# Kernel tuning notes

Hardware: AMD Instinct MI355X
Metric: run time of the kernel (lower is better)

Reference implementation:

```python
import jax, jax.numpy as jnp
import numpy as np

DIM = 3072      # model dim (Qwen-Image)
HEADS = 24
HD = 128        # head dim; inner = HEADS*HD = 3072
INNER = HEADS * HD
FF = 4 * DIM    # 12288
S_IMG = 1024
S_TXT = 256
S_TOT = S_IMG + S_TXT
B = 1
EPS = 1e-6
SCALE_SHIFT = 1.0


def setup_inputs() -> dict:
    key = jax.random.key(0)
    ks = iter(jax.random.split(key, 64))
    W = 0.02

    def nrm(shape, s=W):
        return jax.random.normal(next(ks), shape, dtype=jnp.float32) * s

    # RoPE tables for the joint (txt first, then img) sequence, interleaved layout
    pos = jnp.arange(S_TOT, dtype=jnp.float32)
    inv = 1.0 / (10000.0 ** (jnp.arange(HD // 2, dtype=jnp.float32) / (HD // 2)))
    ang = pos[:, None] * inv[None, :]                       # [S, HD/2]
    rope_cos = jnp.repeat(jnp.cos(ang), 2, axis=-1)         # [S, HD]
    rope_sin = jnp.repeat(jnp.sin(ang), 2, axis=-1)

    inp = {
        "hidden_states": jax.random.normal(next(ks), (B, S_IMG, DIM), dtype=jnp.float32),
        "encoder_hidden_states": jax.random.normal(next(ks), (B, S_TXT, DIM), dtype=jnp.float32),
        "temb": jax.random.normal(next(ks), (B, DIM), dtype=jnp.float32),
        "rope_cos": rope_cos,
        "rope_sin": rope_sin,
        # modulation (AWQW4A16Linear equivalent)
        "img_mod_w": nrm((6 * DIM, DIM)), "img_mod_b": nrm((6 * DIM,)),
        "txt_mod_w": nrm((6 * DIM, DIM)), "txt_mod_b": nrm((6 * DIM,)),
        # attention (SVDQW4A4Linear equivalents)
        "qkv_w": nrm((3 * INNER, DIM)), "qkv_b": nrm((3 * INNER,)),
        "add_qkv_w": nrm((3 * INNER, DIM)), "add_qkv_b": nrm((3 * INNER,)),
        "norm_q_g": jnp.ones((HD,), jnp.float32), "norm_k_g": jnp.ones((HD,), jnp.float32),
        "norm_added_q_g": jnp.ones((HD,), jnp.float32), "norm_added_k_g": jnp.ones((HD,), jnp.float32),
        "to_out_w": nrm((DIM, INNER)), "to_out_b": nrm((DIM,)),
        "to_add_out_w": nrm((DIM, INNER)), "to_add_out_b": nrm((DIM,)),
        # MLPs
        "img_mlp_w1": nrm((FF, DIM)), "img_mlp_b1": nrm((FF,)),
        "img_mlp_w2": nrm((DIM, FF)), "img_mlp_b2": nrm((DIM,)),
        "txt_mlp_w1": nrm((FF, DIM)), "txt_mlp_b1": nrm((FF,)),
        "txt_mlp_w2": nrm((DIM, FF)), "txt_mlp_b2": nrm((DIM,)),
    }
    return inp


def _lin(x, w, b):
    return jnp.matmul(x, w.T) + b


def _ln(x):  # LayerNorm, no affine, eps=1e-6
    mu = jnp.mean(x, axis=-1, keepdims=True)
    var = jnp.mean(jnp.square(x - mu), axis=-1, keepdims=True)
    return (x - mu) * jax.lax.rsqrt(var + EPS)


def _rms(x, g):  # per-head RMSNorm over last dim (HD)
    ms = jnp.mean(jnp.square(x), axis=-1, keepdims=True)
    return x * jax.lax.rsqrt(ms + EPS) * g


def _rope(x, cos, sin):  # x: [B,S,H,D], cos/sin: [S,D], interleaved rotate
    x1 = x[..., 0::2]
    x2 = x[..., 1::2]
    xr = jnp.stack([-x2, x1], axis=-1).reshape(x.shape)
    return x * cos[None, :, None, :] + xr * sin[None, :, None, :]


def _reorder_mod(m):
    # view(B,-1,6).transpose(1,2).reshape(B,-1): de-interleave 6 modulation vecs
    b = m.shape[0]
    return m.reshape(b, DIM, 6).transpose(0, 2, 1).reshape(b, 6 * DIM)


def _modulate(x, mod):
    shift, scale, gate = jnp.split(mod, 3, axis=-1)
    return x * (scale + SCALE_SHIFT)[:, None, :] + shift[:, None, :], gate[:, None, :]


def _mlp(x, w1, b1, w2, b2):  # GELU(tanh) MLP
    h = jax.nn.gelu(_lin(x, w1, b1), approximate=True)
    return _lin(h, w2, b2)


def reference(hidden_states, encoder_hidden_states, temb, rope_cos, rope_sin,
              img_mod_w, img_mod_b, txt_mod_w, txt_mod_b,
              qkv_w, qkv_b, add_qkv_w, add_qkv_b,
              norm_q_g, norm_k_g, norm_added_q_g, norm_added_k_g,
              to_out_w, to_out_b, to_add_out_w, to_add_out_b,
              img_mlp_w1, img_mlp_b1, img_mlp_w2, img_mlp_b2,
              txt_mlp_w1, txt_mlp_b1, txt_mlp_w2, txt_mlp_b2):
    b = hidden_states.shape[0]

    img_mod = _reorder_mod(_lin(jax.nn.silu(temb), img_mod_w, img_mod_b))
    txt_mod = _reorder_mod(_lin(jax.nn.silu(temb), txt_mod_w, txt_mod_b))
    img_mod1, img_mod2 = jnp.split(img_mod, 2, axis=-1)
    txt_mod1, txt_mod2 = jnp.split(txt_mod, 2, axis=-1)

    img_modulated, img_gate1 = _modulate(_ln(hidden_states), img_mod1)
    txt_modulated, txt_gate1 = _modulate(_ln(encoder_hidden_states), txt_mod1)

    # ---- joint attention ----
    img_q, img_k, img_v = jnp.split(_lin(img_modulated, qkv_w, qkv_b), 3, axis=-1)
    txt_q, txt_k, txt_v = jnp.split(_lin(txt_modulated, add_qkv_w, add_qkv_b), 3, axis=-1)

    def heads(x):  # [B,S,INNER] -> [B,S,H,HD]
        return x.reshape(b, x.shape[1], HEADS, HD)

    img_q = _rms(heads(img_q), norm_q_g)
    img_k = _rms(heads(img_k), norm_k_g)
    txt_q = _rms(heads(txt_q), norm_added_q_g)
    txt_k = _rms(heads(txt_k), norm_added_k_g)

    q = jnp.concatenate([txt_q, img_q], axis=1)  # txt first
    k = jnp.concatenate([txt_k, img_k], axis=1)
    v = jnp.concatenate([heads(txt_v), heads(img_v)], axis=1)

    q = _rope(q, rope_cos, rope_sin)
    k = _rope(k, rope_cos, rope_sin)

    scale = 1.0 / jnp.sqrt(jnp.float32(HD))
    scores = jnp.einsum('bqhd,bkhd->bhqk', q, k) * scale
    probs = jax.nn.softmax(scores, axis=-1)
    attn = jnp.einsum('bhqk,bkhd->bqhd', probs, v).reshape(b, S_TOT, INNER)

    txt_attn = attn[:, :S_TXT, :]
    img_attn = attn[:, S_TXT:, :]
    img_attn = _lin(img_attn, to_out_w, to_out_b)
    txt_attn = _lin(txt_attn, to_add_out_w, to_add_out_b)

    hidden_states = hidden_states + img_gate1 * img_attn
    encoder_hidden_states = encoder_hidden_states + txt_gate1 * txt_attn

    # ---- MLPs ----
    img_m2, img_gate2 = _modulate(_ln(hidden_states), img_mod2)
    hidden_states = hidden_states + img_gate2 * _mlp(img_m2, img_mlp_w1, img_mlp_b1, img_mlp_w2, img_mlp_b2)

    txt_m2, txt_gate2 = _modulate(_ln(encoder_hidden_states), txt_mod2)
    encoder_hidden_states = encoder_hidden_states + txt_gate2 * _mlp(txt_m2, txt_mlp_w1, txt_mlp_b1, txt_mlp_w2, txt_mlp_b2)

    return (encoder_hidden_states, hidden_states)
```

## Files before the change

kernel.cpp:

```cpp
#include <hip/hip_runtime.h>

#define DIMC   3072
#define HEADS  24
#define HD     128
#define FF     12288
#define S_IMG  1024
#define S_TXT  256
#define S_TOT  1280
#define EPSF   1e-6f

typedef __attribute__((ext_vector_type(8))) short bf16x8;
typedef __attribute__((ext_vector_type(4))) float f32x4;
typedef __attribute__((ext_vector_type(4))) float float4v;
typedef __attribute__((ext_vector_type(4))) unsigned int u32x4;

__device__ __forceinline__ unsigned short f2bf(float f) {
    union { float f; unsigned u; } c; c.f = f;
    unsigned u = c.u;
    unsigned r = (u + 0x7fffu + ((u >> 16) & 1u)) >> 16;
    return (unsigned short)r;
}
__device__ __forceinline__ float b2f(unsigned short h) {
    union { unsigned u; float f; } c; c.u = ((unsigned)h) << 16;
    return c.f;
}
__device__ __forceinline__ unsigned packbf(float a, float b) {
    union { float f; unsigned u; } x, y; x.f = a; y.f = b;
    return __builtin_amdgcn_perm(y.u + 0x8000u, x.u + 0x8000u, 0x07060302);
}
__device__ __forceinline__ float gelu_tanh(float v) {
    float u = 1.5957691216057308f * (v + 0.044715f * v * v * v);
    float e = __expf(u);
    float t = 1.0f - 2.0f / (e + 1.0f);
    return 0.5f * v * (1.0f + t);
}

#define GLL16(gsrc, ldst)                                                     \
    __builtin_amdgcn_global_load_lds(                                         \
        (const __attribute__((address_space(1))) void*)(gsrc),                \
        (__attribute__((address_space(3))) void*)(ldst), 16, 0, 0)

struct GemmArgs {
    const unsigned short* A;
    const void* B;
    const float* bias;
    void* out;
    long bOut;
};

template<int EPI>
__global__ __launch_bounds__(512, 2)
void gemm_big(GemmArgs g0, GemmArgs g1, int ysplit,
              int K, int lda, int ldb, int ldout)
{
    __shared__ __align__(16) char smem[131072];
    char* smemA = smem;
    char* smemB = smem + 65536;

    const int tid  = threadIdx.x;
    const int lane = tid & 63;
    const int wave = tid >> 6;
    const int wm = wave >> 2, wc = wave & 3;

    const int by = blockIdx.y;
    const bool second = (by >= ysplit);
    const GemmArgs g = second ? g1 : g0;
    const int bm = (second ? by - ysplit : by) * 256;
    const int bn = blockIdx.x * 256;

    const unsigned short* A = g.A;
    const float* Bf = (const float*)g.B;

    const int rA = lane >> 3;
    const int cA = (lane & 7) ^ rA;
    const int pB = tid & 7;
    const int rB0 = tid >> 3;
    const int swB = (rB0 & 7) << 4;

    float4v breg[4][2];

    auto BLOAD = [&](int t) {
        const float* src = Bf + (long)t * 64 + pB * 8;
        #pragma unroll
        for (int i = 0; i < 4; i++) {
            const float* p = src + (long)(bn + rB0 + i * 64) * ldb;
            breg[i][0] = *(const float4v*)p;
            breg[i][1] = *(const float4v*)(p + 4);
        }
    };
    auto ASTAGE = [&](int buf, int t) {
        const long kof = (long)t * 64 + cA * 8;
        #pragma unroll
        for (int i = 0; i < 4; i++) {
            int r = i * 64 + wave * 8 + rA;
            GLL16(A + (long)(bm + r) * lda + kof,
                  smemA + buf * 32768 + i * 8192 + wave * 1024);
        }
    };
    auto BSTORE = [&](int buf) {
        #pragma unroll
        for (int i = 0; i < 4; i++) {
            int r = rB0 + i * 64;
            u32x4 w;
            w[0] = packbf(breg[i][0][0], breg[i][0][1]);
            w[1] = packbf(breg[i][0][2], breg[i][0][3]);
            w[2] = packbf(breg[i][1][0], breg[i][1][1]);
            w[3] = packbf(breg[i][1][2], breg[i][1][3]);
            *(u32x4*)(smemB + buf * 32768 + r * 128 + ((pB * 16) ^ swB)) = w;
        }
    };

    f32x4 acc[8][4] = {};
    auto COMPUTE = [&](int buf) {
        #pragma unroll
        for (int ks = 0; ks < 2; ks++) {
            const int kb = ks * 64 + (lane >> 4) * 16;
            bf16x8 af[8], bfr[4];
            #pragma unroll
            for (int mi = 0; mi < 8; mi++) {
                int r = wm * 128 + mi * 16 + (lane & 15);
                af[mi] = *(const bf16x8*)(smemA + buf * 32768 + r * 128 + (kb ^ ((r & 7) << 4)));
            }
            #pragma unroll
            for (int ni = 0; ni < 4; ni++) {
                int r = wc * 64 + ni * 16 + (lane & 15);
                bfr[ni] = *(const bf16x8*)(smemB + buf * 32768 + r * 128 + (kb ^ ((r & 7) << 4)));
            }
            #pragma unroll
            for (int mi = 0; mi < 8; mi++)
                #pragma unroll
                for (int ni = 0; ni < 4; ni++)
                    acc[mi][ni] = __builtin_amdgcn_mfma_f32_16x16x32_bf16(
                        af[mi], bfr[ni], acc[mi][ni], 0, 0, 0);
        }
    };

    const int nk = K >> 6;
    BLOAD(0);
    ASTAGE(0, 0);
    BSTORE(0);
    __syncthreads();
    for (int t = 0; t < nk; ++t) {
        const int cur = t & 1;
        if (t + 1 < nk) {
            BLOAD(t + 1);
            ASTAGE(cur ^ 1, t + 1);
        }
        __builtin_amdgcn_sched_barrier(0);
        COMPUTE(cur);
        __builtin_amdgcn_sched_barrier(0);
        if (t + 1 < nk) BSTORE(cur ^ 1);
        __syncthreads();
    }

    unsigned short* outh = (unsigned short*)g.out;
    float*          outf = (float*)g.out;
    #pragma unroll
    for (int mi = 0; mi < 8; mi++) {
        #pragma unroll
        for (int ni = 0; ni < 4; ni++) {
            int n = bn + wc * 64 + ni * 16 + (lane & 15);
            float bv = g.bias ? g.bias[n] : 0.0f;
            #pragma unroll
            for (int r = 0; r < 4; r++) {
                int m = bm + wm * 128 + mi * 16 + (lane >> 4) * 4 + r;
                float v = acc[mi][ni][r] + bv;
                long o = (long)m * ldout + n;
                if constexpr (EPI == 0) outf[o] = v;
                else                    outh[o] = f2bf(gelu_tanh(v));
            }
        }
    }
}

template<int EPI, bool BF16B>
__global__ __launch_bounds__(256)
void gemm_bt(GemmArgs g0, GemmArgs g1, int ysplit,
             int K, int lda, int ldb, int ldout,
             long batchA, long batchB)
{
    __shared__ __align__(16) char smem[65536];
    char* smemA = smem;
    char* smemB = smem + 32768;

    const int tid  = threadIdx.x;
    const int lane = tid & 63;
    const int wave = tid >> 6;
    const int wm = wave >> 1, wc = wave & 1;

    const int by = blockIdx.y;
    const bool second = (by >= ysplit);
    const GemmArgs g = second ? g1 : g0;
    const int bm = (second ? by - ysplit : by) * 128;
    const int bn = blockIdx.x * 128;

    const unsigned short* A = g.A + (long)blockIdx.z * batchA;
    const float* Bf = (const float*)g.B + (long)blockIdx.z * batchB;
    const unsigned short* Bh = (const unsigned short*)g.B + (long)blockIdx.z * batchB;

    const int rA = lane >> 3;
    const int cA = (lane & 7) ^ rA;
    const int pB = tid & 7;
    const int rB0 = tid >> 3;
    const int swB = (rB0 & 7) << 4;

    float4v breg[4][2];

    auto BLOAD = [&](int t) {
        const float* src = Bf + (long)t * 64 + pB * 8;
        #pragma unroll
        for (int i = 0; i < 4; i++) {
            const float* p = src + (long)(bn + rB0 + i * 32) * ldb;
            breg[i][0] = *(const float4v*)p;
            breg[i][1] = *(const float4v*)(p + 4);
        }
    };
    auto STAGE_A = [&](int buf, int t) {
        const long kof = (long)t * 64 + cA * 8;
        #pragma unroll
        for (int i = 0; i < 4; i++) {
            int r = i * 32 + wave * 8 + rA;
            GLL16(A + (long)(bm + r) * lda + kof,
                  smemA + buf * 16384 + i * 4096 + wave * 1024);
        }
    };
    auto STAGE_B16 = [&](int buf, int t) {
        const long kof = (long)t * 64 + cA * 8;
        #pragma unroll
        for (int i = 0; i < 4; i++) {
            int r = i * 32 + wave * 8 + rA;
            GLL16(Bh + (long)(bn + r) * ldb + kof,
                  smemB + buf * 16384 + i * 4096 + wave * 1024);
        }
    };
    auto BSTORE = [&](int buf) {
        #pragma unroll
        for (int i = 0; i < 4; i++) {
            int r = rB0 + i * 32;
            u32x4 w;
            w[0] = packbf(breg[i][0][0], breg[i][0][1]);
            w[1] = packbf(breg[i][0][2], breg[i][0][3]);
            w[2] = packbf(breg[i][1][0], breg[i][1][1]);
            w[3] = packbf(breg[i][1][2], breg[i][1][3]);
            *(u32x4*)(smemB + buf * 16384 + r * 128 + ((pB * 16) ^ swB)) = w;
        }
    };

    f32x4 acc[4][4] = {};
    auto COMPUTE = [&](int buf) {
        #pragma unroll
        for (int ks = 0; ks < 2; ks++) {
            const int kb = ks * 64 + (lane >> 4) * 16;
            bf16x8 af[4], bfr[4];
            #pragma unroll
            for (int mi = 0; mi < 4; mi++) {
                int r = wm * 64 + mi * 16 + (lane & 15);
                af[mi] = *(const bf16x8*)(smemA + buf * 16384 + r * 128 + (kb ^ ((r & 7) << 4)));
            }
            #pragma unroll
            for (int ni = 0; ni < 4; ni++) {
                int r = wc * 64 + ni * 16 + (lane & 15);
                bfr[ni] = *(const bf16x8*)(smemB + buf * 16384 + r * 128 + (kb ^ ((r & 7) << 4)));
            }
            #pragma unroll
            for (int mi = 0; mi < 4; mi++)
                #pragma unroll
                for (int ni = 0; ni < 4; ni++)
                    acc[mi][ni] = __builtin_amdgcn_mfma_f32_16x16x32_bf16(
                        af[mi], bfr[ni], acc[mi][ni], 0, 0, 0);
        }
    };

    const int nk = K >> 6;
    if constexpr (BF16B) {
        STAGE_A(0, 0); STAGE_B16(0, 0);
    } else {
        BLOAD(0); STAGE_A(0, 0); BSTORE(0);
    }
    __syncthreads();
    for (int t = 0; t < nk; ++t) {
        const int cur = t & 1;
        if (t + 1 < nk) {
            if constexpr (BF16B) {
                STAGE_A(cur ^ 1, t + 1); STAGE_B16(cur ^ 1, t + 1);
            } else {
                BLOAD(t + 1); STAGE_A(cur ^ 1, t + 1);
            }
        }
        __builtin_amdgcn_sched_barrier(0);
        COMPUTE(cur);
        __builtin_amdgcn_sched_barrier(0);
        if constexpr (!BF16B) { if (t + 1 < nk) BSTORE(cur ^ 1); }
        __syncthreads();
    }

    unsigned short* outh = (unsigned short*)g.out + (long)blockIdx.z * g.bOut;
    float*          outf = (float*)g.out + (long)blockIdx.z * g.bOut;
    #pragma unroll
    for (int mi = 0; mi < 4; mi++) {
        #pragma unroll
        for (int ni = 0; ni < 4; ni++) {
            int n = bn + wc * 64 + ni * 16 + (lane & 15);
            float bv = g.bias ? g.bias[n] : 0.0f;
            #pragma unroll
            for (int r = 0; r < 4; r++) {
                int m = bm + wm * 64 + mi * 16 + (lane >> 4) * 4 + r;
                float v = acc[mi][ni][r] + bv;
                long o = (long)m * ldout + n;
                if constexpr (EPI == 0)      outf[o] = v;
                else                         outh[o] = f2bf(v);
            }
        }
    }
}

__global__ void silu_k(const float* __restrict__ x, float* __restrict__ out) {
    int i = blockIdx.x * 256 + threadIdx.x;
    if (i < DIMC) { float v = x[i]; out[i] = v / (1.0f + expf(-v)); }
}

__global__ __launch_bounds__(256)
void mod_gemv(const float* __restrict__ st,
              const float* __restrict__ Wimg, const float* __restrict__ bimg,
              const float* __restrict__ Wtxt, const float* __restrict__ btxt,
              float* __restrict__ mimg, float* __restrict__ mtxt)
{
    int wv = threadIdx.x >> 6, lane = threadIdx.x & 63;
    int r = blockIdx.x * 4 + wv;
    const float* W = blockIdx.y ? Wtxt : Wimg;
    const float* b = blockIdx.y ? btxt : bimg;
    float* out = blockIdx.y ? mtxt : mimg;
    const float* row = W + (long)r * DIMC;
    float acc = 0.f;
    #pragma unroll
    for (int j = 0; j < 12; j++) {
        float4v wvv = ((const float4v*)row)[lane + j * 64];
        float4v xv  = ((const float4v*)st)[lane + j * 64];
        acc += wvv[0] * xv[0] + wvv[1] * xv[1] + wvv[2] * xv[2] + wvv[3] * xv[3];
    }
    #pragma unroll
    for (int o = 32; o; o >>= 1) acc += __shfl_xor(acc, o);
    if (lane == 0) {
        int d = r / 6, j6 = r % 6;
        out[j6 * DIMC + d] = acc + b[r];
    }
}

__global__ __launch_bounds__(256)
void ln_mod(const float* __restrict__ x, const float* __restrict__ shift,
            const float* __restrict__ scale, unsigned short* __restrict__ out)
{
    __shared__ float red[8];
    long row = blockIdx.x;
    const float* xr = x + row * DIMC;
    float4v v[3];
    float sum = 0.f, sq = 0.f;
    #pragma unroll
    for (int j = 0; j < 3; j++) {
        v[j] = ((const float4v*)xr)[threadIdx.x + j * 256];
        #pragma unroll
        for (int c = 0; c < 4; c++) { sum += v[j][c]; sq += v[j][c] * v[j][c]; }
    }
    int lane = threadIdx.x & 63, wv = threadIdx.x >> 6;
// ... 37 lines not shown
        float4v q1 = ((const float4v*)(p1 + off))[idx];
        float4v gb = ((const float4v*)pbias)[idx];
        float4v gt = ((const float4v*)gate1)[idx];
        #pragma unroll
        for (int c = 0; c < 4; c++) {
            float val = a[c] + gt[c] * (gb[c] + q0[c] + q1[c]);
            v[j][c] = val; sum += val; sq += val * val;
        }
        ((float4v*)(h1 + off))[idx] = v[j];
    }
    int lane = threadIdx.x & 63, wv = threadIdx.x >> 6;
    #pragma unroll
    for (int o = 32; o; o >>= 1) { sum += __shfl_xor(sum, o); sq += __shfl_xor(sq, o); }
    if (lane == 0) { red[wv] = sum; red[4 + wv] = sq; }
    __syncthreads();
    sum = red[0] + red[1] + red[2] + red[3];
    sq  = red[4] + red[5] + red[6] + red[7];
    float mu = sum / DIMC;
    float rstd = rsqrtf(sq / DIMC - mu * mu + EPSF);
    #pragma unroll
    for (int j = 0; j < 3; j++) {
        int nb = (threadIdx.x + j * 256) * 4;
        #pragma unroll
        for (int c = 0; c < 4; c++) {
            int n = nb + c;
            float y = (v[j][c] - mu) * rstd * (scale2[n] + 1.0f) + shift2[n];
            mA[off + n] = f2bf(y);
        }
    }
}

__global__ __launch_bounds__(256)
void reduce_out(const float* __restrict__ p, long PS,
                const float* __restrict__ h1, const float* __restrict__ wbias,
                const float* __restrict__ gate2, float* __restrict__ out, int n4)
{
    int i = blockIdx.x * 256 + threadIdx.x;
    if (i >= n4) return;
    int n = (i * 4) % DIMC;
    float4v s = ((const float4v*)p)[i];
    float4v s1 = ((const float4v*)(p + PS))[i];
    float4v s2 = ((const float4v*)(p + 2 * PS))[i];
    float4v s3 = ((const float4v*)(p + 3 * PS))[i];
    float4v h = ((const float4v*)h1)[i];
    float4v bv = *(const float4v*)(wbias + n);
    float4v gv = *(const float4v*)(gate2 + n);
    float4v r;
    #pragma unroll
    for (int c = 0; c < 4; c++)
        r[c] = h[c] + gv[c] * (bv[c] + s[c] + s1[c] + s2[c] + s3[c]);
    ((float4v*)out)[i] = r;
}

__global__ __launch_bounds__(64)
void qkv_post(const float* __restrict__ qkv_img, const float* __restrict__ qkv_txt,
              const float* __restrict__ nqg, const float* __restrict__ nkg,
              const float* __restrict__ naqg, const float* __restrict__ nakg,
              const float* __restrict__ rc, const float* __restrict__ rs,
              unsigned short* __restrict__ q, unsigned short* __restrict__ k,
              unsigned short* __restrict__ vt)
{
    int s = blockIdx.x;
    int h = blockIdx.y;
    int d0 = threadIdx.x;
    const float *src, *gq, *gk;
    if (s < S_TXT) { src = qkv_txt + (long)s * 3 * DIMC; gq = naqg; gk = nakg; }
    else           { src = qkv_img + (long)(s - S_TXT) * 3 * DIMC; gq = nqg; gk = nkg; }

    float q0 = src[h * HD + d0],            q1 = src[h * HD + d0 + 64];
    float k0 = src[DIMC + h * HD + d0],     k1 = src[DIMC + h * HD + d0 + 64];
    float v0 = src[2 * DIMC + h * HD + d0], v1 = src[2 * DIMC + h * HD + d0 + 64];

    float sqq = q0 * q0 + q1 * q1;
    float sqk = k0 * k0 + k1 * k1;
    #pragma unroll
    for (int o = 32; o; o >>= 1) { sqq += __shfl_xor(sqq, o); sqk += __shfl_xor(sqk, o); }
    float rq = rsqrtf(sqq / (float)HD + EPSF);
    float rk = rsqrtf(sqk / (float)HD + EPSF);
    q0 *= rq * gq[d0]; q1 *= rq * gq[d0 + 64];
    k0 *= rk * gk[d0]; k1 *= rk * gk[d0 + 64];

    float qp0 = __shfl_xor(q0, 1), qp1 = __shfl_xor(q1, 1);
    float kp0 = __shfl_xor(k0, 1), kp1 = __shfl_xor(k1, 1);
    float c0 = rc[(long)s * HD + d0], c1 = rc[(long)s * HD + d0 + 64];
    float s0 = rs[(long)s * HD + d0], s1 = rs[(long)s * HD + d0 + 64];
    float sgn = (d0 & 1) ? 1.0f : -1.0f;
    float qo0 = q0 * c0 + sgn * qp0 * s0;
    float qo1 = q1 * c1 + sgn * qp1 * s1;
    float ko0 = k0 * c0 + sgn * kp0 * s0;
    float ko1 = k1 * c1 + sgn * kp1 * s1;

    const float scl = 0.08838834764831845f;
    long qkbase = ((long)h * S_TOT + s) * HD;
    q[qkbase + d0]      = f2bf(qo0 * scl);
    q[qkbase + d0 + 64] = f2bf(qo1 * scl);
    k[qkbase + d0]      = f2bf(ko0);
    k[qkbase + d0 + 64] = f2bf(ko1);
    vt[((long)h * HD + d0) * S_TOT + s]        = f2bf(v0);
    vt[((long)h * HD + d0 + 64) * S_TOT + s]   = f2bf(v1);
}

__global__ __launch_bounds__(256)
void softmax_k(unsigned short* __restrict__ scores)
{
    long row = (long)blockIdx.x * 4 + (threadIdx.x >> 6);
    int lane = threadIdx.x & 63;
    unsigned short* p = scores + row * S_TOT;
    float v[20];
    float mx = -1e30f;
    #pragma unroll
    for (int j = 0; j < 20; j++) { v[j] = b2f(p[lane + j * 64]); mx = fmaxf(mx, v[j]); }
    #pragma unroll
    for (int o = 32; o; o >>= 1) mx = fmaxf(mx, __shfl_xor(mx, o));
    float sum = 0.f;
    #pragma unroll
    for (int j = 0; j < 20; j++) { v[j] = __expf(v[j] - mx); sum += v[j]; }
    #pragma unroll
    for (int o = 32; o; o >>= 1) sum += __shfl_xor(sum, o);
    float inv = 1.0f / sum;
    #pragma unroll
    for (int j = 0; j < 20; j++) p[lane + j * 64] = f2bf(v[j] * inv);
}

extern "C" void kernel_launch(void* const* d_in, const int* in_sizes, int n_in,
                              void* d_out, int out_size, void* d_ws, size_t ws_size,
                              hipStream_t stream)
{
    const float* hidden   = (const float*)d_in[0];
    const float* enc      = (const float*)d_in[1];
    const float* temb     = (const float*)d_in[2];
    const float* rope_cos = (const float*)d_in[3];
    const float* rope_sin = (const float*)d_in[4];
    const float* img_mod_w = (const float*)d_in[5];
    const float* img_mod_b = (const float*)d_in[6];
    const float* txt_mod_w = (const float*)d_in[7];
    const float* txt_mod_b = (const float*)d_in[8];
    const float* qkv_w     = (const float*)d_in[9];
    const float* qkv_b     = (const float*)d_in[10];
    const float* add_qkv_w = (const float*)d_in[11];
    const float* add_qkv_b = (const float*)d_in[12];
    const float* norm_q_g  = (const float*)d_in[13];
    const float* norm_k_g  = (const float*)d_in[14];
    const float* norm_aq_g = (const float*)d_in[15];
    const float* norm_ak_g = (const float*)d_in[16];
    const float* to_out_w  = (const float*)d_in[17];
    const float* to_out_b  = (const float*)d_in[18];
    const float* to_add_out_w = (const float*)d_in[19];
    const float* to_add_out_b = (const float*)d_in[20];
    const float* img_mlp_w1 = (const float*)d_in[21];
    const float* img_mlp_b1 = (const float*)d_in[22];
    const float* img_mlp_w2 = (const float*)d_in[23];
    const float* img_mlp_b2 = (const float*)d_in[24];
    const float* txt_mlp_w1 = (const float*)d_in[25];
    const float* txt_mlp_b1 = (const float*)d_in[26];
    const float* txt_mlp_w2 = (const float*)d_in[27];
    const float* txt_mlp_b2 = (const float*)d_in[28];

    char* w = (char*)d_ws;
    auto alloc = [&](size_t bytes) { char* p = w; w += (bytes + 255) & ~(size_t)255; return p; };
    float* silu_t  = (float*)alloc(DIMC * 4);
    float* mod_img = (float*)alloc(6 * DIMC * 4);
    float* mod_txt = (float*)alloc(6 * DIMC * 4);
    unsigned short* mA_img = (unsigned short*)alloc((long)S_IMG * DIMC * 2);
    unsigned short* mA_txt = (unsigned short*)alloc((long)S_TXT * DIMC * 2);
    float* qkv_img = (float*)alloc((long)S_IMG * 3 * DIMC * 4);
    float* qkv_txt = (float*)alloc((long)S_TXT * 3 * DIMC * 4);
    unsigned short* qb = (unsigned short*)alloc((long)HEADS * S_TOT * HD * 2);
    unsigned short* kb = (unsigned short*)alloc((long)HEADS * S_TOT * HD * 2);
    unsigned short* vt = (unsigned short*)alloc((long)HEADS * HD * S_TOT * 2);
    unsigned short* scores = (unsigned short*)alloc((long)HEADS * S_TOT * S_TOT * 2);
    unsigned short* attn = (unsigned short*)alloc((long)S_TOT * DIMC * 2);
    float* h1_img = (float*)alloc((long)S_IMG * DIMC * 4);
    float* h1_txt = (float*)alloc((long)S_TXT * DIMC * 4);
    unsigned short* gelu_img = (unsigned short*)alloc((long)S_IMG * FF * 2);
    unsigned short* gelu_txt = (unsigned short*)alloc((long)S_TXT * FF * 2);

    const long PS = (long)S_TOT * DIMC;
    float* part = (float*)scores;
    float* part_img = part;
    float* part_txt = part + (long)S_IMG * DIMC;

    float* out_enc = (float*)d_out;
    float* out_hid = (float*)d_out + (long)S_TXT * DIMC;

    silu_k<<<12, 256, 0, stream>>>(temb, silu_t);
    mod_gemv<<<dim3(4608, 2), 256, 0, stream>>>(silu_t, img_mod_w, img_mod_b,
                                                txt_mod_w, txt_mod_b, mod_img, mod_txt);

    ln_mod<<<S_IMG, 256, 0, stream>>>(hidden, mod_img, mod_img + DIMC, mA_img);
    ln_mod<<<S_TXT, 256, 0, stream>>>(enc, mod_txt, mod_txt + DIMC, mA_txt);

    {
        GemmArgs gi{mA_img, qkv_w, qkv_b, qkv_img, 0};
        GemmArgs gt{mA_txt, add_qkv_w, add_qkv_b, qkv_txt, 0};
        gemm_big<0><<<dim3(36, 5), 512, 0, stream>>>(
            gi, gt, 4, DIMC, DIMC, DIMC, 3 * DIMC);
    }

    qkv_post<<<dim3(S_TOT, HEADS), 64, 0, stream>>>(
        qkv_img, qkv_txt, norm_q_g, norm_k_g, norm_aq_g, norm_ak_g,
        rope_cos, rope_sin, qb, kb, vt);

    {
        GemmArgs gs{qb, kb, nullptr, scores, (long)S_TOT * S_TOT};
        gemm_bt<1, true><<<dim3(10, 10, HEADS), 256, 0, stream>>>(
            gs, gs, 10, HD, HD, HD, S_TOT,
            (long)S_TOT * HD, (long)S_TOT * HD);
    }
    softmax_k<<<(HEADS * S_TOT) / 4, 256, 0, stream>>>(scores);
    {
        GemmArgs gp{scores, vt, nullptr, attn, HD};
        gemm_bt<1, true><<<dim3(1, 10, HEADS), 256, 0, stream>>>(
            gp, gp, 10, S_TOT, S_TOT, S_TOT, DIMC,
            (long)S_TOT * S_TOT, (long)HD * S_TOT);
    }

    {
        GemmArgs gi{attn + (long)S_TXT * DIMC, to_out_w, nullptr, part_img, PS};
        GemmArgs gt{attn, to_add_out_w, nullptr, part_txt, PS};
        gemm_bt<0, false><<<dim3(24, 10, 2), 256, 0, stream>>>(
            gi, gt, 8, 1536, DIMC, DIMC, DIMC, 1536, 1536);
    }

    reduce_ln<<<S_IMG, 256, 0, stream>>>(
        part_img, part_img + PS, to_out_b, hidden,
        mod_img + 2 * DIMC, mod_img + 3 * DIMC, mod_img + 4 * DIMC,
        h1_img, mA_img);
    reduce_ln<<<S_TXT, 256, 0, stream>>>(
        part_txt, part_txt + PS, to_add_out_b, enc,
        mod_txt + 2 * DIMC, mod_txt + 3 * DIMC, mod_txt + 4 * DIMC,
        h1_txt, mA_txt);

    {
        GemmArgs gi{mA_img, img_mlp_w1, img_mlp_b1, gelu_img, 0};
        GemmArgs gt{mA_txt, txt_mlp_w1, txt_mlp_b1, gelu_txt, 0};
        gemm_big<2><<<dim3(48, 5), 512, 0, stream>>>(
            gi, gt, 4, DIMC, DIMC, DIMC, FF);
    }

    {
        GemmArgs gi{gelu_img, img_mlp_w2, nullptr, part_img, PS};
        GemmArgs gt{gelu_txt, txt_mlp_w2, nullptr, part_txt, PS};
        gemm_bt<0, false><<<dim3(24, 10, 4), 256, 0, stream>>>(
            gi, gt, 8, 3072, FF, FF, DIMC, 3072, 3072);
    }
    reduce_out<<<(S_IMG * DIMC / 4 + 255) / 256, 256, 0, stream>>>(
        part_img, PS, h1_img, img_mlp_b2, mod_img + 5 * DIMC, out_hid,
        S_IMG * DIMC / 4);
    reduce_out<<<(S_TXT * DIMC / 4 + 255) / 256, 256, 0, stream>>>(
        part_txt, PS, h1_txt, txt_mlp_b2, mod_txt + 5 * DIMC, out_enc,
        S_TXT * DIMC / 4);
}
```

Before: 765.0 us.

## Swap GEMM operands and stage bf16 output tile through LDS for coalesced stores

```diff
diff --git a/kernel.cpp b/kernel.cpp
--- a/kernel.cpp
+++ b/kernel.cpp
@@ -13,6 +13,7 @@
 typedef __attribute__((ext_vector_type(4))) float f32x4;
 typedef __attribute__((ext_vector_type(4))) float float4v;
 typedef __attribute__((ext_vector_type(4))) unsigned int u32x4;
+typedef __attribute__((ext_vector_type(2))) unsigned int u32x2;
 
 __device__ __forceinline__ unsigned short f2bf(float f) {
     union { float f; unsigned u; } c; c.f = f;
@@ -39,6 +40,149 @@
     __builtin_amdgcn_global_load_lds(                                         \
         (const __attribute__((address_space(1))) void*)(gsrc),                \
         (__attribute__((address_space(3))) void*)(ldst), 16, 0, 0)
+
+struct SwpArgs {
+    const float* W;
+    const unsigned short* X;
+    const float* bias;
+    unsigned short* out;
+};
+
+template<int EPI>
+__global__ __launch_bounds__(512, 2)
+void gemm_swp(SwpArgs g0, SwpArgs g1, int ysplit, int K, int ldout)
+{
+    __shared__ __align__(16) char smem[131072];
+    char* smemW = smem;
+    char* smemX = smem + 65536;
+
+    const int tid  = threadIdx.x;
+    const int lane = tid & 63;
+    const int wave = tid >> 6;
+    const int wm = wave >> 2, wc = wave & 3;
+
+    const int by = blockIdx.y;
+    const bool second = (by >= ysplit);
+    const SwpArgs g = second ? g1 : g0;
+    const int sTile = (second ? by - ysplit : by) * 256;
+    const int bm = blockIdx.x * 256;
+
+    const int pW  = tid & 7;
+    const int rW0 = tid >> 3;
+    const int swW = (rW0 & 7) << 4;
+    const int rX = lane >> 3;
+    const int cX = (lane & 7) ^ rX;
+
+    float4v wreg[4][2];
+
+    auto WLOAD = [&](int t) {
+        const float* src = g.W + (long)t * 64 + pW * 8;
+        #pragma unroll
+        for (int i = 0; i < 4; i++) {
+            const float* p = src + (long)(bm + rW0 + i * 64) * K;
+            wreg[i][0] = *(const float4v*)p;
+            wreg[i][1] = *(const float4v*)(p + 4);
+        }
+    };
+    auto WSTORE = [&](int buf) {
+        #pragma unroll
+        for (int i = 0; i < 4; i++) {
+            int r = rW0 + i * 64;
+            u32x4 w;
+            w[0] = packbf(wreg[i][0][0], wreg[i][0][1]);
+            w[1] = packbf(wreg[i][0][2], wreg[i][0][3]);
+            w[2] = packbf(wreg[i][1][0], wreg[i][1][1]);
+            w[3] = packbf(wreg[i][1][2], wreg[i][1][3]);
+            *(u32x4*)(smemW + buf * 32768 + r * 128 + ((pW * 16) ^ swW)) = w;
+        }
+    };
+    auto XSTAGE = [&](int buf, int t) {
+        const long kof = (long)t * 64 + cX * 8;
+        #pragma unroll
+        for (int i = 0; i < 4; i++) {
+            int r = i * 64 + wave * 8 + rX;
+            GLL16(g.X + (long)(sTile + r) * K + kof,
+                  smemX + buf * 32768 + i * 8192 + wave * 1024);
+        }
+    };
+
+    f32x4 acc[8][4] = {};
+    auto COMPUTE = [&](int buf) {
+        #pragma unroll
+        for (int ks = 0; ks < 2; ks++) {
+            const int kb = ks * 64 + (lane >> 4) * 16;
+            bf16x8 wf[8], xf[4];
+            #pragma unroll
+            for (int mi = 0; mi < 8; mi++) {
+                int r = wm * 128 + mi * 16 + (lane & 15);
+                wf[mi] = *(const bf16x8*)(smemW + buf * 32768 + r * 128 + (kb ^ ((r & 7) << 4)));
+            }
+            #pragma unroll
+            for (int ni = 0; ni < 4; ni++) {
+                int r = wc * 64 + ni * 16 + (lane & 15);
+                xf[ni] = *(const bf16x8*)(smemX + buf * 32768 + r * 128 + (kb ^ ((r & 7) << 4)));
+            }
+            #pragma unroll
+            for (int mi = 0; mi < 8; mi++)
+                #pragma unroll
+                for (int ni = 0; ni < 4; ni++)
+                    acc[mi][ni] = __builtin_amdgcn_mfma_f32_16x16x32_bf16(
+                        wf[mi], xf[ni], acc[mi][ni], 0, 0, 0);
+        }
+    };
+
+    const int nk = K >> 6;
+    WLOAD(0);
+    XSTAGE(0, 0);
+    WSTORE(0);
+    __syncthreads();
+    for (int t = 0; t < nk; ++t) {
+        const int cur = t & 1;
+        if (t + 1 < nk) {
+            WLOAD(t + 1);
+            XSTAGE(cur ^ 1, t + 1);
+        }
+        __builtin_amdgcn_sched_barrier(0);
+        COMPUTE(cur);
+        __builtin_amdgcn_sched_barrier(0);
+        if (t + 1 < nk) WSTORE(cur ^ 1);
+        __syncthreads();
+    }
+
+    #pragma unroll
+    for (int mi = 0; mi < 8; mi++) {
+        int m0 = wm * 128 + mi * 16 + ((lane >> 4) << 2);
+        float4v bv = *(const float4v*)(g.bias + bm + m0);
+        #pragma unroll
+        for (int ni = 0; ni < 4; ni++) {
+            int n = wc * 64 + ni * 16 + (lane & 15);
+            float v0 = acc[mi][ni][0] + bv[0];
+            float v1 = acc[mi][ni][1] + bv[1];
+            float v2 = acc[mi][ni][2] + bv[2];
+            float v3 = acc[mi][ni][3] + bv[3];
+            if constexpr (EPI == 2) {
+                v0 = gelu_tanh(v0); v1 = gelu_tanh(v1);
+                v2 = gelu_tanh(v2); v3 = gelu_tanh(v3);
+            }
+            u32x2 w;
+            w[0] = packbf(v0, v1);
+            w[1] = packbf(v2, v3);
+            *(u32x2*)(smem + n * 512 + ((2 * m0) ^ ((n & 31) << 4))) = w;
+        }
+    }
+    __syncthreads();
+    {
+        const int s = tid >> 1;
+        const int cbase = (tid & 1) * 16;
+        unsigned short* orow = g.out + (long)(sTile + s) * ldout + bm;
+        #pragma unroll
+        for (int c = 0; c < 16; c++) {
+            int chunk = cbase + c;
+            u32x4 d = *(const u32x4*)(smem + s * 512 + ((chunk * 16) ^ ((s & 31) << 4)));
+            *(u32x4*)(orow + chunk * 8) = d;
+        }
+    }
+}
 
 struct GemmArgs {
     const unsigned short* A;
@@ -47,131 +191,6 @@
     void* out;
     long bOut;
 };
-
-template<int EPI>
-__global__ __launch_bounds__(512, 2)
-void gemm_big(GemmArgs g0, GemmArgs g1, int ysplit,
-              int K, int lda, int ldb, int ldout)
-{
-    __shared__ __align__(16) char smem[131072];
-    char* smemA = smem;
-    char* smemB = smem + 65536;
-
-    const int tid  = threadIdx.x;
-    const int lane = tid & 63;
-    const int wave = tid >> 6;
-    const int wm = wave >> 2, wc = wave & 3;
-
-    const int by = blockIdx.y;
-    const bool second = (by >= ysplit);
-    const GemmArgs g = second ? g1 : g0;
-    const int bm = (second ? by - ysplit : by) * 256;
-    const int bn = blockIdx.x * 256;
-
-    const unsigned short* A = g.A;
-    const float* Bf = (const float*)g.B;
-
-    const int rA = lane >> 3;
-    const int cA = (lane & 7) ^ rA;
-    const int pB = tid & 7;
-    const int rB0 = tid >> 3;
-    const int swB = (rB0 & 7) << 4;
-
-    float4v breg[4][2];
-
-    auto BLOAD = [&](int t) {
-        const float* src = Bf + (long)t * 64 + pB * 8;
-        #pragma unroll
-        for (int i = 0; i < 4; i++) {
-            const float* p = src + (long)(bn + rB0 + i * 64) * ldb;
-            breg[i][0] = *(const float4v*)p;
-            breg[i][1] = *(const float4v*)(p + 4);
-        }
-    };
-    auto ASTAGE = [&](int buf, int t) {
-        const long kof = (long)t * 64 + cA * 8;
-        #pragma unroll
-        for (int i = 0; i < 4; i++) {
-            int r = i * 64 + wave * 8 + rA;
-            GLL16(A + (long)(bm + r) * lda + kof,
-                  smemA + buf * 32768 + i * 8192 + wave * 1024);
-        }
-    };
-    auto BSTORE = [&](int buf) {
-        #pragma unroll
-        for (int i = 0; i < 4; i++) {
-            int r = rB0 + i * 64;
-            u32x4 w;
-            w[0] = packbf(breg[i][0][0], breg[i][0][1]);
-            w[1] = packbf(breg[i][0][2], breg[i][0][3]);
-            w[2] = packbf(breg[i][1][0], breg[i][1][1]);
-            w[3] = packbf(breg[i][1][2], breg[i][1][3]);
-            *(u32x4*)(smemB + buf * 32768 + r * 128 + ((pB * 16) ^ swB)) = w;
-        }
-    };
-
-    f32x4 acc[8][4] = {};
-    auto COMPUTE = [&](int buf) {
-        #pragma unroll
-        for (int ks = 0; ks < 2; ks++) {
-            const int kb = ks * 64 + (lane >> 4) * 16;
-            bf16x8 af[8], bfr[4];
-            #pragma unroll
-            for (int mi = 0; mi < 8; mi++) {
-                int r = wm * 128 + mi * 16 + (lane & 15);
-                af[mi] = *(const bf16x8*)(smemA + buf * 32768 + r * 128 + (kb ^ ((r & 7) << 4)));
-            }
-            #pragma unroll
-            for (int ni = 0; ni < 4; ni++) {
-                int r = wc * 64 + ni * 16 + (lane & 15);
-                bfr[ni] = *(const bf16x8*)(smemB + buf * 32768 + r * 128 + (kb ^ ((r & 7) << 4)));
-            }
-            #pragma unroll
-            for (int mi = 0; mi < 8; mi++)
-                #pragma unroll
-                for (int ni = 0; ni < 4; ni++)
-                    acc[mi][ni] = __builtin_amdgcn_mfma_f32_16x16x32_bf16(
-                        af[mi], bfr[ni], acc[mi][ni], 0, 0, 0);
-        }
-    };
-
-    const int nk = K >> 6;
-    BLOAD(0);
-    ASTAGE(0, 0);
-    BSTORE(0);
-    __syncthreads();
-    for (int t = 0; t < nk; ++t) {
-        const int cur = t & 1;
-        if (t + 1 < nk) {
-            BLOAD(t + 1);
-            ASTAGE(cur ^ 1, t + 1);
-        }
-        __builtin_amdgcn_sched_barrier(0);
-        COMPUTE(cur);
-        __builtin_amdgcn_sched_barrier(0);
-        if (t + 1 < nk) BSTORE(cur ^ 1);
-        __syncthreads();
-    }
-
-    unsigned short* outh = (unsigned short*)g.out;
-    float*          outf = (float*)g.out;
-    #pragma unroll
-    for (int mi = 0; mi < 8; mi++) {
-        #pragma unroll
-        for (int ni = 0; ni < 4; ni++) {
-            int n = bn + wc * 64 + ni * 16 + (lane & 15);
-            float bv = g.bias ? g.bias[n] : 0.0f;
-            #pragma unroll
-            for (int r = 0; r < 4; r++) {
-                int m = bm + wm * 128 + mi * 16 + (lane >> 4) * 4 + r;
-                float v = acc[mi][ni][r] + bv;
-                long o = (long)m * ldout + n;
-                if constexpr (EPI == 0) outf[o] = v;
-                else                    outh[o] = f2bf(gelu_tanh(v));
-            }
-        }
-    }
-}
 
 template<int EPI, bool BF16B>
 __global__ __launch_bounds__(256)
@@ -452,8 +471,9 @@
     ((float4v*)out)[i] = r;
 }
 
-__global__ __launch_bounds__(64)
-void qkv_post(const float* __restrict__ qkv_img, const float* __restrict__ qkv_txt,
+__global__ __launch_bounds__(256)
+void qkv_post(const unsigned short* __restrict__ qkv_img,
+              const unsigned short* __restrict__ qkv_txt,
               const float* __restrict__ nqg, const float* __restrict__ nkg,
               const float* __restrict__ naqg, const float* __restrict__ nakg,
               const float* __restrict__ rc, const float* __restrict__ rs,
@@ -461,15 +481,16 @@
               unsigned short* __restrict__ vt)
 {
     int s = blockIdx.x;
-    int h = blockIdx.y;
-    int d0 = threadIdx.x;
-    const float *src, *gq, *gk;
+    int h = blockIdx.y * 4 + (threadIdx.x >> 6);
+    int d0 = threadIdx.x & 63;
+    const unsigned short* src;
+    const float *gq, *gk;
     if (s < S_TXT) { src = qkv_txt + (long)s * 3 * DIMC; gq = naqg; gk = nakg; }
     else           { src = qkv_img + (long)(s - S_TXT) * 3 * DIMC; gq = nqg; gk = nkg; }
 
-    float q0 = src[h * HD + d0],            q1 = src[h * HD + d0 + 64];
-    float k0 = src[DIMC + h * HD + d0],     k1 = src[DIMC + h * HD + d0 + 64];
-    float v0 = src[2 * DIMC + h * HD + d0], v1 = src[2 * DIMC + h * HD + d0 + 64];
+    float q0 = b2f(src[h * HD + d0]),            q1 = b2f(src[h * HD + d0 + 64]);
+    float k0 = b2f(src[DIMC + h * HD + d0]),     k1 = b2f(src[DIMC + h * HD + d0 + 64]);
+    float v0 = b2f(src[2 * DIMC + h * HD + d0]), v1 = b2f(src[2 * DIMC + h * HD + d0 + 64]);
 
     float sqq = q0 * q0 + q1 * q1;
     float sqk = k0 * k0 + k1 * k1;
@@ -563,8 +584,8 @@
     float* mod_txt = (float*)alloc(6 * DIMC * 4);
     unsigned short* mA_img = (unsigned short*)alloc((long)S_IMG * DIMC * 2);
     unsigned short* mA_txt = (unsigned short*)alloc((long)S_TXT * DIMC * 2);
-    float* qkv_img = (float*)alloc((long)S_IMG * 3 * DIMC * 4);
-    float* qkv_txt = (float*)alloc((long)S_TXT * 3 * DIMC * 4);
+    unsigned short* qkv_img = (unsigned short*)alloc((long)S_IMG * 3 * DIMC * 2);
+    unsigned short* qkv_txt = (unsigned short*)alloc((long)S_TXT * 3 * DIMC * 2);
     unsigned short* qb = (unsigned short*)alloc((long)HEADS * S_TOT * HD * 2);
     unsigned short* kb = (unsigned short*)alloc((long)HEADS * S_TOT * HD * 2);
     unsigned short* vt = (unsigned short*)alloc((long)HEADS * HD * S_TOT * 2);
@@ -591,13 +612,12 @@
     ln_mod<<<S_TXT, 256, 0, stream>>>(enc, mod_txt, mod_txt + DIMC, mA_txt);
 
     {
-        GemmArgs gi{mA_img, qkv_w, qkv_b, qkv_img, 0};
-        GemmArgs gt{mA_txt, add_qkv_w, add_qkv_b, qkv_txt, 0};
-        gemm_big<0><<<dim3(36, 5), 512, 0, stream>>>(
-            gi, gt, 4, DIMC, DIMC, DIMC, 3 * DIMC);
-    }
-
-    qkv_post<<<dim3(S_TOT, HEADS), 64, 0, stream>>>(
+        SwpArgs gi{qkv_w, mA_img, qkv_b, qkv_img};
+        SwpArgs gt{add_qkv_w, mA_txt, add_qkv_b, qkv_txt};
+        gemm_swp<1><<<dim3(36, 5), 512, 0, stream>>>(gi, gt, 4, DIMC, 3 * DIMC);
+    }
+
+    qkv_post<<<dim3(S_TOT, HEADS / 4), 256, 0, stream>>>(
         qkv_img, qkv_txt, norm_q_g, norm_k_g, norm_aq_g, norm_ak_g,
         rope_cos, rope_sin, qb, kb, vt);
 
@@ -632,10 +652,9 @@
         h1_txt, mA_txt);
 
     {
-        GemmArgs gi{mA_img, img_mlp_w1, img_mlp_b1, gelu_img, 0};
-        GemmArgs gt{mA_txt, txt_mlp_w1, txt_mlp_b1, gelu_txt, 0};
-        gemm_big<2><<<dim3(48, 5), 512, 0, stream>>>(
-            gi, gt, 4, DIMC, DIMC, DIMC, FF);
+        SwpArgs gi{img_mlp_w1, mA_img, img_mlp_b1, gelu_img};
+        SwpArgs gt{txt_mlp_w1, mA_txt, txt_mlp_b1, gelu_txt};
+        gemm_swp<2><<<dim3(48, 5), 512, 0, stream>>>(gi, gt, 4, DIMC, FF);
     }
 
     {
```

Measured after the change: 767.7 us. No clear change (+0.4%).

## Replace 256-tile GEMMs with XCD-aware 128-tile GEMM, bf16 QKV output

Applied to the files above, without the earlier changes.

```diff
diff --git a/kernel.cpp b/kernel.cpp
--- a/kernel.cpp
+++ b/kernel.cpp
@@ -49,27 +49,35 @@
 };
 
 template<int EPI>
-__global__ __launch_bounds__(512, 2)
-void gemm_big(GemmArgs g0, GemmArgs g1, int ysplit,
-              int K, int lda, int ldb, int ldout)
-{
-    __shared__ __align__(16) char smem[131072];
+__global__ __launch_bounds__(256)
+void gemm_bt(GemmArgs g0, GemmArgs g1, int ysplit,
+             int K, int lda, int ldb, int ldout,
+             long batchA, long batchB, int nbn)
+{
+    const int id = blockIdx.x;
+    const int xcd = id & 7, t = id >> 3;
+    const int by = t % 10;
+    const int slot = t / 10;
+    const int gidx = slot * 8 + xcd;
+    const int bnIdx = gidx % nbn;
+    const int z = gidx / nbn;
+
+    __shared__ __align__(16) char smem[65536];
     char* smemA = smem;
-    char* smemB = smem + 65536;
+    char* smemB = smem + 32768;
 
     const int tid  = threadIdx.x;
     const int lane = tid & 63;
     const int wave = tid >> 6;
-    const int wm = wave >> 2, wc = wave & 3;
-
-    const int by = blockIdx.y;
+    const int wm = wave >> 1, wc = wave & 1;
+
     const bool second = (by >= ysplit);
     const GemmArgs g = second ? g1 : g0;
-    const int bm = (second ? by - ysplit : by) * 256;
-    const int bn = blockIdx.x * 256;
-
-    const unsigned short* A = g.A;
-    const float* Bf = (const float*)g.B;
+    const int bm = (second ? by - ysplit : by) * 128;
+    const int bn = bnIdx * 128;
+
+    const unsigned short* A = g.A + (long)z * batchA;
+    const float* Bf = (const float*)g.B + (long)z * batchB;
 
     const int rA = lane >> 3;
     const int cA = (lane & 7) ^ rA;
@@ -83,133 +91,6 @@
         const float* src = Bf + (long)t * 64 + pB * 8;
         #pragma unroll
         for (int i = 0; i < 4; i++) {
-            const float* p = src + (long)(bn + rB0 + i * 64) * ldb;
-            breg[i][0] = *(const float4v*)p;
-            breg[i][1] = *(const float4v*)(p + 4);
-        }
-    };
-    auto ASTAGE = [&](int buf, int t) {
-        const long kof = (long)t * 64 + cA * 8;
-        #pragma unroll
-        for (int i = 0; i < 4; i++) {
-            int r = i * 64 + wave * 8 + rA;
-            GLL16(A + (long)(bm + r) * lda + kof,
-                  smemA + buf * 32768 + i * 8192 + wave * 1024);
-        }
-    };
-    auto BSTORE = [&](int buf) {
-        #pragma unroll
-        for (int i = 0; i < 4; i++) {
-            int r = rB0 + i * 64;
-            u32x4 w;
-            w[0] = packbf(breg[i][0][0], breg[i][0][1]);
-            w[1] = packbf(breg[i][0][2], breg[i][0][3]);
-            w[2] = packbf(breg[i][1][0], breg[i][1][1]);
-            w[3] = packbf(breg[i][1][2], breg[i][1][3]);
-            *(u32x4*)(smemB + buf * 32768 + r * 128 + ((pB * 16) ^ swB)) = w;
-        }
-    };
-
-    f32x4 acc[8][4] = {};
-    auto COMPUTE = [&](int buf) {
-        #pragma unroll
-        for (int ks = 0; ks < 2; ks++) {
-            const int kb = ks * 64 + (lane >> 4) * 16;
-            bf16x8 af[8], bfr[4];
-            #pragma unroll
-            for (int mi = 0; mi < 8; mi++) {
-                int r = wm * 128 + mi * 16 + (lane & 15);
-                af[mi] = *(const bf16x8*)(smemA + buf * 32768 + r * 128 + (kb ^ ((r & 7) << 4)));
-            }
-            #pragma unroll
-            for (int ni = 0; ni < 4; ni++) {
-                int r = wc * 64 + ni * 16 + (lane & 15);
-                bfr[ni] = *(const bf16x8*)(smemB + buf * 32768 + r * 128 + (kb ^ ((r & 7) << 4)));
-            }
-            #pragma unroll
-            for (int mi = 0; mi < 8; mi++)
-                #pragma unroll
-                for (int ni = 0; ni < 4; ni++)
-                    acc[mi][ni] = __builtin_amdgcn_mfma_f32_16x16x32_bf16(
-                        af[mi], bfr[ni], acc[mi][ni], 0, 0, 0);
-        }
-    };
-
-    const int nk = K >> 6;
-    BLOAD(0);
-    ASTAGE(0, 0);
-    BSTORE(0);
-    __syncthreads();
-    for (int t = 0; t < nk; ++t) {
-        const int cur = t & 1;
-        if (t + 1 < nk) {
-            BLOAD(t + 1);
-            ASTAGE(cur ^ 1, t + 1);
-        }
-        __builtin_amdgcn_sched_barrier(0);
-        COMPUTE(cur);
-        __builtin_amdgcn_sched_barrier(0);
-        if (t + 1 < nk) BSTORE(cur ^ 1);
-        __syncthreads();
-    }
-
-    unsigned short* outh = (unsigned short*)g.out;
-    float*          outf = (float*)g.out;
-    #pragma unroll
-    for (int mi = 0; mi < 8; mi++) {
-        #pragma unroll
-        for (int ni = 0; ni < 4; ni++) {
-            int n = bn + wc * 64 + ni * 16 + (lane & 15);
-            float bv = g.bias ? g.bias[n] : 0.0f;
-            #pragma unroll
-            for (int r = 0; r < 4; r++) {
-                int m = bm + wm * 128 + mi * 16 + (lane >> 4) * 4 + r;
-                float v = acc[mi][ni][r] + bv;
-                long o = (long)m * ldout + n;
-                if constexpr (EPI == 0) outf[o] = v;
-                else                    outh[o] = f2bf(gelu_tanh(v));
-            }
-        }
-    }
-}
-
-template<int EPI, bool BF16B>
-__global__ __launch_bounds__(256)
-void gemm_bt(GemmArgs g0, GemmArgs g1, int ysplit,
-             int K, int lda, int ldb, int ldout,
-             long batchA, long batchB)
-{
-    __shared__ __align__(16) char smem[65536];
-    char* smemA = smem;
-    char* smemB = smem + 32768;
-
-    const int tid  = threadIdx.x;
-    const int lane = tid & 63;
-    const int wave = tid >> 6;
-    const int wm = wave >> 1, wc = wave & 1;
-
-    const int by = blockIdx.y;
-    const bool second = (by >= ysplit);
-    const GemmArgs g = second ? g1 : g0;
-    const int bm = (second ? by - ysplit : by) * 128;
-    const int bn = blockIdx.x * 128;
-
-    const unsigned short* A = g.A + (long)blockIdx.z * batchA;
-    const float* Bf = (const float*)g.B + (long)blockIdx.z * batchB;
-    const unsigned short* Bh = (const unsigned short*)g.B + (long)blockIdx.z * batchB;
-
-    const int rA = lane >> 3;
-    const int cA = (lane & 7) ^ rA;
-    const int pB = tid & 7;
-    const int rB0 = tid >> 3;
-    const int swB = (rB0 & 7) << 4;
-
-    float4v breg[4][2];
-
-    auto BLOAD = [&](int t) {
-        const float* src = Bf + (long)t * 64 + pB * 8;
-        #pragma unroll
-        for (int i = 0; i < 4; i++) {
             const float* p = src + (long)(bn + rB0 + i * 32) * ldb;
             breg[i][0] = *(const float4v*)p;
             breg[i][1] = *(const float4v*)(p + 4);
@@ -222,15 +103,6 @@
             int r = i * 32 + wave * 8 + rA;
             GLL16(A + (long)(bm + r) * lda + kof,
                   smemA + buf * 16384 + i * 4096 + wave * 1024);
-        }
-    };
-    auto STAGE_B16 = [&](int buf, int t) {
-        const long kof = (long)t * 64 + cA * 8;
-        #pragma unroll
-        for (int i = 0; i < 4; i++) {
-            int r = i * 32 + wave * 8 + rA;
-            GLL16(Bh + (long)(bn + r) * ldb + kof,
-                  smemB + buf * 16384 + i * 4096 + wave * 1024);
         }
     };
     auto BSTORE = [&](int buf) {
@@ -272,30 +144,22 @@
     };
 
     const int nk = K >> 6;
-    if constexpr (BF16B) {
-        STAGE_A(0, 0); STAGE_B16(0, 0);
-    } else {
-        BLOAD(0); STAGE_A(0, 0); BSTORE(0);
-    }
+    BLOAD(0); STAGE_A(0, 0); BSTORE(0);
     __syncthreads();
     for (int t = 0; t < nk; ++t) {
         const int cur = t & 1;
         if (t + 1 < nk) {
-            if constexpr (BF16B) {
-                STAGE_A(cur ^ 1, t + 1); STAGE_B16(cur ^ 1, t + 1);
-            } else {
-                BLOAD(t + 1); STAGE_A(cur ^ 1, t + 1);
-            }
+            BLOAD(t + 1); STAGE_A(cur ^ 1, t + 1);
         }
         __builtin_amdgcn_sched_barrier(0);
         COMPUTE(cur);
         __builtin_amdgcn_sched_barrier(0);
-        if constexpr (!BF16B) { if (t + 1 < nk) BSTORE(cur ^ 1); }
+        if (t + 1 < nk) BSTORE(cur ^ 1);
         __syncthreads();
     }
 
-    unsigned short* outh = (unsigned short*)g.out + (long)blockIdx.z * g.bOut;
-    float*          outf = (float*)g.out + (long)blockIdx.z * g.bOut;
+    unsigned short* outh = (unsigned short*)g.out + (long)z * g.bOut;
+    float*          outf = (float*)g.out + (long)z * g.bOut;
     #pragma unroll
     for (int mi = 0; mi < 4; mi++) {
         #pragma unroll
@@ -308,7 +172,110 @@
                 float v = acc[mi][ni][r] + bv;
                 long o = (long)m * ldout + n;
                 if constexpr (EPI == 0)      outf[o] = v;
-                else                         outh[o] = f2bf(v);
+                else if constexpr (EPI == 1) outh[o] = f2bf(v);
+                else                         outh[o] = f2bf(gelu_tanh(v));
+            }
+        }
+    }
+}
+
+struct AttArgs {
+    const unsigned short* A;
+    const unsigned short* B;
+    unsigned short* out;
+    long bOut;
+};
+
+__global__ __launch_bounds__(256)
+void gemm_att(AttArgs g, int K, int lda, int ldb, int ldout,
+              long batchA, long batchB)
+{
+    const int by = blockIdx.y, bnIdx = blockIdx.x, z = blockIdx.z;
+
+    __shared__ __align__(16) char smem[65536];
+    char* smemA = smem;
+    char* smemB = smem + 32768;
+
+    const int tid  = threadIdx.x;
+    const int lane = tid & 63;
+    const int wave = tid >> 6;
+    const int wm = wave >> 1, wc = wave & 1;
+
+    const int bm = by * 128;
+    const int bn = bnIdx * 128;
+
+    const unsigned short* A = g.A + (long)z * batchA;
+    const unsigned short* Bh = g.B + (long)z * batchB;
+
+    const int rA = lane >> 3;
+    const int cA = (lane & 7) ^ rA;
+
+    auto STAGE_A = [&](int buf, int t) {
+        const long kof = (long)t * 64 + cA * 8;
+        #pragma unroll
+        for (int i = 0; i < 4; i++) {
+            int r = i * 32 + wave * 8 + rA;
+            GLL16(A + (long)(bm + r) * lda + kof,
+                  smemA + buf * 16384 + i * 4096 + wave * 1024);
+        }
+    };
+    auto STAGE_B = [&](int buf, int t) {
+        const long kof = (long)t * 64 + cA * 8;
+        #pragma unroll
+        for (int i = 0; i < 4; i++) {
+            int r = i * 32 + wave * 8 + rA;
+            GLL16(Bh + (long)(bn + r) * ldb + kof,
+                  smemB + buf * 16384 + i * 4096 + wave * 1024);
+        }
+    };
+
+    f32x4 acc[4][4] = {};
+    auto COMPUTE = [&](int buf) {
+        #pragma unroll
+        for (int ks = 0; ks < 2; ks++) {
+            const int kb = ks * 64 + (lane >> 4) * 16;
+            bf16x8 af[4], bfr[4];
+            #pragma unroll
+            for (int mi = 0; mi < 4; mi++) {
+                int r = wm * 64 + mi * 16 + (lane & 15);
+                af[mi] = *(const bf16x8*)(smemA + buf * 16384 + r * 128 + (kb ^ ((r & 7) << 4)));
+            }
+            #pragma unroll
+            for (int ni = 0; ni < 4; ni++) {
+                int r = wc * 64 + ni * 16 + (lane & 15);
+                bfr[ni] = *(const bf16x8*)(smemB + buf * 16384 + r * 128 + (kb ^ ((r & 7) << 4)));
+            }
+            #pragma unroll
+            for (int mi = 0; mi < 4; mi++)
+                #pragma unroll
+                for (int ni = 0; ni < 4; ni++)
+                    acc[mi][ni] = __builtin_amdgcn_mfma_f32_16x16x32_bf16(
+                        af[mi], bfr[ni], acc[mi][ni], 0, 0, 0);
+        }
+    };
+
+    const int nk = K >> 6;
+    STAGE_A(0, 0); STAGE_B(0, 0);
+    __syncthreads();
+    for (int t = 0; t < nk; ++t) {
+        const int cur = t & 1;
+        if (t + 1 < nk) { STAGE_A(cur ^ 1, t + 1); STAGE_B(cur ^ 1, t + 1); }
+        __builtin_amdgcn_sched_barrier(0);
+        COMPUTE(cur);
+        __builtin_amdgcn_sched_barrier(0);
+        __syncthreads();
+    }
+
+    unsigned short* outh = g.out + (long)z * g.bOut;
+    #pragma unroll
+    for (int mi = 0; mi < 4; mi++) {
+        #pragma unroll
+        for (int ni = 0; ni < 4; ni++) {
+            int n = bn + wc * 64 + ni * 16 + (lane & 15);
+            #pragma unroll
+            for (int r = 0; r < 4; r++) {
+                int m = bm + wm * 64 + mi * 16 + (lane >> 4) * 4 + r;
+                outh[(long)m * ldout + n] = f2bf(acc[mi][ni][r]);
             }
         }
     }
@@ -452,8 +419,9 @@
     ((float4v*)out)[i] = r;
 }
 
-__global__ __launch_bounds__(64)
-void qkv_post(const float* __restrict__ qkv_img, const float* __restrict__ qkv_txt,
+__global__ __launch_bounds__(256)
+void qkv_post(const unsigned short* __restrict__ qkv_img,
+              const unsigned short* __restrict__ qkv_txt,
               const float* __restrict__ nqg, const float* __restrict__ nkg,
               const float* __restrict__ naqg, const float* __restrict__ nakg,
               const float* __restrict__ rc, const float* __restrict__ rs,
@@ -461,15 +429,16 @@
               unsigned short* __restrict__ vt)
 {
     int s = blockIdx.x;
-    int h = blockIdx.y;
-    int d0 = threadIdx.x;
-    const float *src, *gq, *gk;
+    int h = blockIdx.y * 4 + (threadIdx.x >> 6);
+    int d0 = threadIdx.x & 63;
+    const unsigned short* src;
+    const float *gq, *gk;
     if (s < S_TXT) { src = qkv_txt + (long)s * 3 * DIMC; gq = naqg; gk = nakg; }
     else           { src = qkv_img + (long)(s - S_TXT) * 3 * DIMC; gq = nqg; gk = nkg; }
 
-    float q0 = src[h * HD + d0],            q1 = src[h * HD + d0 + 64];
-    float k0 = src[DIMC + h * HD + d0],     k1 = src[DIMC + h * HD + d0 + 64];
-    float v0 = src[2 * DIMC + h * HD + d0], v1 = src[2 * DIMC + h * HD + d0 + 64];
+    float q0 = b2f(src[h * HD + d0]),            q1 = b2f(src[h * HD + d0 + 64]);
+    float k0 = b2f(src[DIMC + h * HD + d0]),     k1 = b2f(src[DIMC + h * HD + d0 + 64]);
+    float v0 = b2f(src[2 * DIMC + h * HD + d0]), v1 = b2f(src[2 * DIMC + h * HD + d0 + 64]);
 
     float sqq = q0 * q0 + q1 * q1;
     float sqk = k0 * k0 + k1 * k1;
@@ -563,8 +532,8 @@
     float* mod_txt = (float*)alloc(6 * DIMC * 4);
     unsigned short* mA_img = (unsigned short*)alloc((long)S_IMG * DIMC * 2);
     unsigned short* mA_txt = (unsigned short*)alloc((long)S_TXT * DIMC * 2);
-    float* qkv_img = (float*)alloc((long)S_IMG * 3 * DIMC * 4);
-    float* qkv_txt = (float*)alloc((long)S_TXT * 3 * DIMC * 4);
+    unsigned short* qkv_img = (unsigned short*)alloc((long)S_IMG * 3 * DIMC * 2);
+    unsigned short* qkv_txt = (unsigned short*)alloc((long)S_TXT * 3 * DIMC * 2);
     unsigned short* qb = (unsigned short*)alloc((long)HEADS * S_TOT * HD * 2);
     unsigned short* kb = (unsigned short*)alloc((long)HEADS * S_TOT * HD * 2);
     unsigned short* vt = (unsigned short*)alloc((long)HEADS * HD * S_TOT * 2);
@@ -593,33 +562,32 @@
     {
         GemmArgs gi{mA_img, qkv_w, qkv_b, qkv_img, 0};
         GemmArgs gt{mA_txt, add_qkv_w, add_qkv_b, qkv_txt, 0};
-        gemm_big<0><<<dim3(36, 5), 512, 0, stream>>>(
-            gi, gt, 4, DIMC, DIMC, DIMC, 3 * DIMC);
-    }
-
-    qkv_post<<<dim3(S_TOT, HEADS), 64, 0, stream>>>(
+        gemm_bt<1><<<72 * 10, 256, 0, stream>>>(
+            gi, gt, 8, DIMC, DIMC, DIMC, 3 * DIMC, 0, 0, 72);
+    }
+
+    qkv_post<<<dim3(S_TOT, HEADS / 4), 256, 0, stream>>>(
         qkv_img, qkv_txt, norm_q_g, norm_k_g, norm_aq_g, norm_ak_g,
         rope_cos, rope_sin, qb, kb, vt);
 
     {
-        GemmArgs gs{qb, kb, nullptr, scores, (long)S_TOT * S_TOT};
-        gemm_bt<1, true><<<dim3(10, 10, HEADS), 256, 0, stream>>>(
-            gs, gs, 10, HD, HD, HD, S_TOT,
-            (long)S_TOT * HD, (long)S_TOT * HD);
+        AttArgs gs{qb, kb, scores, (long)S_TOT * S_TOT};
+        gemm_att<<<dim3(10, 10, HEADS), 256, 0, stream>>>(
+            gs, HD, HD, HD, S_TOT, (long)S_TOT * HD, (long)S_TOT * HD);
     }
     softmax_k<<<(HEADS * S_TOT) / 4, 256, 0, stream>>>(scores);
     {
-        GemmArgs gp{scores, vt, nullptr, attn, HD};
-        gemm_bt<1, true><<<dim3(1, 10, HEADS), 256, 0, stream>>>(
-            gp, gp, 10, S_TOT, S_TOT, S_TOT, DIMC,
+        AttArgs gp{scores, vt, attn, HD};
+        gemm_att<<<dim3(1, 10, HEADS), 256, 0, stream>>>(
+            gp, S_TOT, S_TOT, S_TOT, DIMC,
             (long)S_TOT * S_TOT, (long)HD * S_TOT);
     }
 
     {
         GemmArgs gi{attn + (long)S_TXT * DIMC, to_out_w, nullptr, part_img, PS};
         GemmArgs gt{attn, to_add_out_w, nullptr, part_txt, PS};
-        gemm_bt<0, false><<<dim3(24, 10, 2), 256, 0, stream>>>(
-            gi, gt, 8, 1536, DIMC, DIMC, DIMC, 1536, 1536);
+        gemm_bt<0><<<24 * 2 * 10, 256, 0, stream>>>(
+            gi, gt, 8, 1536, DIMC, DIMC, DIMC, 1536, 1536, 24);
     }
 
     reduce_ln<<<S_IMG, 256, 0, stream>>>(
@@ -634,15 +602,15 @@
     {
         GemmArgs gi{mA_img, img_mlp_w1, img_mlp_b1, gelu_img, 0};
         GemmArgs gt{mA_txt, txt_mlp_w1, txt_mlp_b1, gelu_txt, 0};
-        gemm_big<2><<<dim3(48, 5), 512, 0, stream>>>(
-            gi, gt, 4, DIMC, DIMC, DIMC, FF);
+        gemm_bt<2><<<96 * 10, 256, 0, stream>>>(
+            gi, gt, 8, DIMC, DIMC, DIMC, FF, 0, 0, 96);
     }
 
     {
         GemmArgs gi{gelu_img, img_mlp_w2, nullptr, part_img, PS};
         GemmArgs gt{gelu_txt, txt_mlp_w2, nullptr, part_txt, PS};
-        gemm_bt<0, false><<<dim3(24, 10, 4), 256, 0, stream>>>(
-            gi, gt, 8, 3072, FF, FF, DIMC, 3072, 3072);
+        gemm_bt<0><<<24 * 4 * 10, 256, 0, stream>>>(
+            gi, gt, 8, 3072, FF, FF, DIMC, 3072, 3072, 24);
     }
     reduce_out<<<(S_IMG * DIMC / 4 + 255) / 256, 256, 0, stream>>>(
         part_img, PS, h1_img, img_mlp_b2, mod_img + 5 * DIMC, out_hid,
```

Measured after the change: 810.7 us. 1.06x slower.
